# Performance work log

Measured on AMD Instinct MI355X. Metric: run time of the kernel, lower is better.

## Reference

```python
import jax, jax.numpy as jnp
import numpy as np

D = 1024
H = 16
HD = D // H
EPS = 1e-5
NEG = -1e20


def _layernorm(x, w, b):
    m = jnp.mean(x, axis=-1, keepdims=True)
    v = jnp.mean((x - m) ** 2, axis=-1, keepdims=True)
    return (x - m) * jax.lax.rsqrt(v + EPS) * w + b


def setup_inputs() -> dict:
    key = jax.random.key(0)
    ks = jax.random.split(key, 16)
    s = 0.02
    inp = {
        "X": jax.random.normal(ks[0], (2, 2048, D), jnp.float32),
        "Wq": jax.random.normal(ks[1], (D, D), jnp.float32) * s,
        "bq": jnp.zeros((D,), jnp.float32),
        "Wk": jax.random.normal(ks[2], (D, D), jnp.float32) * s,
        "bk": jnp.zeros((D,), jnp.float32),
        "Wv": jax.random.normal(ks[3], (D, D), jnp.float32) * s,
        "bv": jnp.zeros((D,), jnp.float32),
        "Wo": jax.random.normal(ks[4], (D, D), jnp.float32) * s,
        "bo": jnp.zeros((D,), jnp.float32),
        "ln1_w": jnp.ones((D,), jnp.float32),
        "ln1_b": jnp.zeros((D,), jnp.float32),
        "Wup": jax.random.normal(ks[5], (4 * D, D), jnp.float32) * s,
        "bup": jnp.zeros((4 * D,), jnp.float32),
        "Wdown": jax.random.normal(ks[6], (D, 4 * D), jnp.float32) * s,
        "bdown": jnp.zeros((D,), jnp.float32),
        "ln2_w": jnp.ones((D,), jnp.float32),
        "ln2_b": jnp.zeros((D,), jnp.float32),
    }
    return inp


def reference(X, Wq, bq, Wk, bk, Wv, bv, Wo, bo, ln1_w, ln1_b,
              Wup, bup, Wdown, bdown, ln2_w, ln2_b):
    B, S, _ = X.shape
    # QKV projections -> [B, H, S, HD]
    q = (X @ Wq.T + bq).reshape(B, S, H, HD).transpose(0, 2, 1, 3)
    k = (X @ Wk.T + bk).reshape(B, S, H, HD).transpose(0, 2, 1, 3)
    v = (X @ Wv.T + bv).reshape(B, S, H, HD).transpose(0, 2, 1, 3)
    scores = jnp.einsum("bhqd,bhkd->bhqk", q, k) / jnp.sqrt(jnp.float32(HD))
    causal = jnp.tril(jnp.ones((S, S), dtype=bool))  # mask==0 -> -1e20
    scores = jnp.where(causal, scores, jnp.float32(NEG))
    attn = jax.nn.softmax(scores, axis=-1)  # dropout is identity in eval
    out = jnp.einsum("bhqk,bhkd->bhqd", attn, v)
    out = out.transpose(0, 2, 1, 3).reshape(B, S, D)
    out = out @ Wo.T + bo
    x = _layernorm(X + out, ln1_w, ln1_b)  # post-LN attention block
    up = jax.nn.relu(x @ Wup.T + bup)
    down = up @ Wdown.T + bdown
    return _layernorm(x + down, ln2_w, ln2_b)
```

## Files before the change

### kernel.cpp

```cpp
#include <hip/hip_runtime.h>
#include <stdint.h>

#define DMODEL 1024
#define NHEAD 16
#define HDIM 64
#define SEQ 2048
#define NBATCH 2
#define MTOK 4096

typedef float f32x4 __attribute__((ext_vector_type(4)));
typedef short s16x8 __attribute__((ext_vector_type(8)));
typedef unsigned short u16;
typedef u16 u16x4 __attribute__((ext_vector_type(4)));

typedef __attribute__((address_space(1))) const void* as1_cvp;
typedef __attribute__((address_space(3))) void* as3_vp;

__device__ inline u16 f2bf(float f) {
  uint32_t u = __float_as_uint(f);
  u = u + 0x7FFFu + ((u >> 16) & 1u);
  return (u16)(u >> 16);
}

__device__ inline uint32_t pk_bf16(float lo, float hi) {
  uint32_t r;
  asm("v_cvt_pk_bf16_f32 %0, %1, %2" : "=v"(r) : "v"(lo), "v"(hi));
  return r;
}

__device__ inline void gload_lds16(const void* g, void* l) {
  __builtin_amdgcn_global_load_lds((as1_cvp)g, (as3_vp)l, 16, 0, 0);
}

__global__ __launch_bounds__(256) void k_f2bf_all(
    const float* __restrict__ X, const float* __restrict__ Wq,
    const float* __restrict__ Wk, const float* __restrict__ Wv,
    const float* __restrict__ Wo, const float* __restrict__ Wup,
    const float* __restrict__ Wdown, u16* __restrict__ dX,
    u16* __restrict__ dqkv, u16* __restrict__ dwo, u16* __restrict__ dup,
    u16* __restrict__ ddown) {
  const int c = blockIdx.y;
  const size_t CH = 1024 * 1024;
  const float* src;
  u16* dst;
  if (c < 4) {
    src = X + c * CH; dst = dX + c * CH;
  } else if (c < 7) {
    src = (c == 4 ? Wq : c == 5 ? Wk : Wv) ; dst = dqkv + (size_t)(c - 4) * CH;
  } else if (c == 7) {
    src = Wo; dst = dwo;
  } else if (c < 12) {
    src = Wup + (size_t)(c - 8) * CH; dst = dup + (size_t)(c - 8) * CH;
  } else {
    src = Wdown + (size_t)(c - 12) * CH; dst = ddown + (size_t)(c - 12) * CH;
  }
  const int n4 = (int)(CH / 4);
  int i = blockIdx.x * 256 + threadIdx.x;
  const int stride = gridDim.x * 256;
  for (; i < n4; i += stride) {
    f32x4 v = ((const f32x4*)src)[i];
    u16x4 o;
    o[0] = f2bf(v[0]); o[1] = f2bf(v[1]); o[2] = f2bf(v[2]); o[3] = f2bf(v[3]);
    ((u16x4*)dst)[i] = o;
  }
}

template <int MODE, int KSPL, int MH>
__global__ __launch_bounds__(512, 2) void k_gemm256(
    const u16* __restrict__ A, const u16* __restrict__ B,
    const float* __restrict__ bias, void* __restrict__ Cv,
    void* __restrict__ Cv1, int M, int N, int K) {
  constexpr int HALVES = MH + 2;
  __shared__ alignas(16) u16 lds[2 * HALVES * 8192];
  const int t = threadIdx.x;
  const int w = t >> 6;
  const int l = t & 63;
  const int wr = w >> 2;
  const int wc = w & 3;
  const int lr = l & 15, lg = l >> 4;
  const int r7 = lr & 7;
  const int lrow8 = l >> 3;

  const int gx = gridDim.x;
  int lin = blockIdx.y * gx + blockIdx.x;
  const int nwg = gx * gridDim.y;
  lin = (lin & 7) * (nwg >> 3) + (lin >> 3);
  const int bx = lin % gx, by = lin / gx;
  const int kz = KSPL > 1 ? blockIdx.z : 0;
  const int Kc = K / KSPL, kbeg = kz * Kc;
  const int brow = by * (MH * 128), bcol = bx * 256;

  constexpr int MF = MH * 4;
  const f32x4 Z4 = {0.f, 0.f, 0.f, 0.f};
  f32x4 acc[MF][4];
#pragma unroll
  for (int m = 0; m < MF; m++)
#pragma unroll
    for (int n = 0; n < 4; n++) acc[m][n] = Z4;

  const u16* Ag = A + (size_t)brow * K + kbeg;
  const u16* Bg = B + (size_t)bcol * K + kbeg;
  const int swz_src = ((l & 7) ^ ((l >> 3) & 7)) << 3;

  auto ldsH = [&](int buf, int half) { return lds + (buf * HALVES + half) * 8192; };
  auto stageA = [&](int kt, int buf) {
#pragma unroll
    for (int h = 0; h < MH; h++) {
      u16* lb = ldsH(buf, h);
      const int rb = h * 128;
      gload_lds16(Ag + (size_t)(rb + w * 8 + lrow8) * K + kt * 64 + swz_src,
                  lb + w * 512);
      gload_lds16(Ag + (size_t)(rb + 64 + w * 8 + lrow8) * K + kt * 64 + swz_src,
                  lb + (8 + w) * 512);
    }
  };
  auto stageB = [&](int kt, int buf) {
#pragma unroll
    for (int h = 0; h < 2; h++) {
      u16* lb = ldsH(buf, MH + h);
      const int rb = h * 128;
      gload_lds16(Bg + (size_t)(rb + w * 8 + lrow8) * K + kt * 64 + swz_src,
                  lb + w * 512);
      gload_lds16(Bg + (size_t)(rb + 64 + w * 8 + lrow8) * K + kt * 64 + swz_src,
                  lb + (8 + w) * 512);
    }
  };

  stageA(0, 0);
  stageB(0, 0);

  const int nkt = Kc >> 6;
  const int arb = (MH == 2) ? 0 : wr * 64;
  const int brb = (wc & 1) * 64;
  for (int kt = 0; kt < nkt; ++kt) {
    const int cur = kt & 1, nx = cur ^ 1;
    if (kt + 1 < nkt) {
      stageA(kt + 1, nx);
      if (MH == 2)
        asm volatile("s_waitcnt vmcnt(4)" ::: "memory");
      else
        asm volatile("s_waitcnt vmcnt(2)" ::: "memory");
    } else {
      asm volatile("s_waitcnt vmcnt(0)" ::: "memory");
    }
    __builtin_amdgcn_s_barrier();
    __builtin_amdgcn_sched_barrier(0);
    const u16* Ah = ldsH(cur, (MH == 2) ? wr : 0);
    const u16* Bh = ldsH(cur, MH + (wc >> 1));
#pragma unroll
    for (int kk = 0; kk < 2; kk++) {
      s16x8 bfr[4];
#pragma unroll
      for (int nf = 0; nf < 4; nf++)
        bfr[nf] = *(const s16x8*)(Bh + (brb + nf * 16 + lr) * 64 +
                                  (((kk * 4 + lg) ^ r7) << 3));
#pragma unroll
      for (int mh = 0; mh < MH; mh++) {
        s16x8 afr[4];
#pragma unroll
        for (int i = 0; i < 4; i++)
          afr[i] = *(const s16x8*)(Ah + (arb + (mh * 4 + i) * 16 + lr) * 64 +
                                   (((kk * 4 + lg) ^ r7) << 3));
        __builtin_amdgcn_s_setprio(1);
#pragma unroll
        for (int i = 0; i < 4; i++)
#pragma unroll
          for (int nf = 0; nf < 4; nf++)
            acc[mh * 4 + i][nf] = __builtin_amdgcn_mfma_f32_16x16x32_bf16(
                afr[i], bfr[nf], acc[mh * 4 + i][nf], 0, 0, 0);
        __builtin_amdgcn_s_setprio(0);
      }
      if (kk == 0 && kt + 1 < nkt) stageB(kt + 1, nx);
    }
    __builtin_amdgcn_sched_barrier(0);
    __builtin_amdgcn_s_barrier();
  }

  const int lg4 = lg * 4;
  const int wrb = wr * (MH == 2 ? 128 : 64);
  if (MODE == 0) {
    float* Co = (kz == 0) ? (float*)Cv : (float*)Cv1;
#pragma unroll
    for (int nf = 0; nf < 4; nf++) {
      const int col = bcol + wc * 64 + nf * 16 + lr;
      const float bvv = (kz == 0) ? bias[col] : 0.0f;
#pragma unroll
      for (int mf = 0; mf < MF; mf++) {
        const int row0 = brow + wrb + mf * 16 + lg4;
#pragma unroll
        for (int r = 0; r < 4; r++)
          Co[(size_t)(row0 + r) * N + col] = acc[mf][nf][r] + bvv;
      }
    }
  } else {
    u16* Sgw = lds + w * 2176;
    float bn[4];
#pragma unroll
    for (int nf = 0; nf < 4; nf++) bn[nf] = bias[bcol + wc * 64 + nf * 16 + lr];
    const int ch = l & 7;
#pragma unroll
    for (int hh = 0; hh < MH * 2; hh++) {
#pragma unroll
      for (int mm = 0; mm < 2; mm++) {
        const int mf = hh * 2 + mm;
#pragma unroll
        for (int nf = 0; nf < 4; nf++)
#pragma unroll
          for (int r = 0; r < 4; r++) {
            float vv = acc[mf][nf][r] + bn[nf];
            if (MODE == 2) vv = vv > 0.f ? vv : 0.f;
            Sgw[(mm * 16 + lg4 + r) * 68 + nf * 16 + lr] = f2bf(vv);
          }
      }
#pragma unroll
      for (int i = 0; i < 4; i++) {
        const int rr = i * 8 + (l >> 3);
        u16x4 a0 = *(const u16x4*)(Sgw + rr * 68 + ch * 8);
        u16x4 a1 = *(const u16x4*)(Sgw + rr * 68 + ch * 8 + 4);
        s16x8 v8;
#pragma unroll
        for (int j = 0; j < 4; j++) { v8[j] = (short)a0[j]; v8[4 + j] = (short)a1[j]; }
        *(s16x8*)((u16*)Cv + (size_t)(brow + wrb + hh * 32 + rr) * N +
                  (bcol + wc * 64 + ch * 8)) = v8;
      }
    }
  }
}

__global__ __launch_bounds__(512, 2) void k_gemm256_qkv(
    const u16* __restrict__ A, const u16* __restrict__ B,
    const float* __restrict__ bq, const float* __restrict__ bk,
    const float* __restrict__ bv, u16* __restrict__ qbf, u16* __restrict__ kbf,
    u16* __restrict__ vtbf, int M, int N, int K) {
  __shared__ alignas(16) u16 lds[2 * 4 * 8192];
  const int t = threadIdx.x;
  const int w = t >> 6, l = t & 63;
  const int wr = w >> 2, wc = w & 3;
  const int lr = l & 15, lg = l >> 4;
  const int r7 = lr & 7;
  const int lrow8 = l >> 3;

  const int gx = gridDim.x;
  int lin = blockIdx.y * gx + blockIdx.x;
  const int nwg = gx * gridDim.y;
  lin = (lin & 7) * (nwg >> 3) + (lin >> 3);
  const int bx = lin % gx, by = lin / gx;
  const int brow = by * 256, bcol = bx * 256;

  const f32x4 Z4 = {0.f, 0.f, 0.f, 0.f};
  f32x4 acc[8][4];
#pragma unroll
  for (int m = 0; m < 8; m++)
#pragma unroll
    for (int n = 0; n < 4; n++) acc[m][n] = Z4;

  const u16* Ag = A + (size_t)brow * K;
  const u16* Bg = B + (size_t)bcol * K;
  const int swz_src = ((l & 7) ^ ((l >> 3) & 7)) << 3;

  auto ldsH = [&](int buf, int half) { return lds + (buf * 4 + half) * 8192; };
  auto stageA = [&](int kt, int buf) {
#pragma unroll
    for (int h = 0; h < 2; h++) {
      u16* lb = ldsH(buf, h);
      const int rb = h * 128;
      gload_lds16(Ag + (size_t)(rb + w * 8 + lrow8) * K + kt * 64 + swz_src,
                  lb + w * 512);
      gload_lds16(Ag + (size_t)(rb + 64 + w * 8 + lrow8) * K + kt * 64 + swz_src,
                  lb + (8 + w) * 512);
    }
  };
  auto stageB = [&](int kt, int buf) {
#pragma unroll
    for (int h = 0; h < 2; h++) {
      u16* lb = ldsH(buf, 2 + h);
      const int rb = h * 128;
      gload_lds16(Bg + (size_t)(rb + w * 8 + lrow8) * K + kt * 64 + swz_src,
                  lb + w * 512);
      gload_lds16(Bg + (size_t)(rb + 64 + w * 8 + lrow8) * K + kt * 64 + swz_src,
                  lb + (8 + w) * 512);
    }
  };

  stageA(0, 0);
  stageB(0, 0);

  const int nkt = K >> 6;
  const int brb = (wc & 1) * 64;
  for (int kt = 0; kt < nkt; ++kt) {
    const int cur = kt & 1, nx = cur ^ 1;
    if (kt + 1 < nkt) {
      stageA(kt + 1, nx);
      asm volatile("s_waitcnt vmcnt(4)" ::: "memory");
    } else {
      asm volatile("s_waitcnt vmcnt(0)" ::: "memory");
    }
    __builtin_amdgcn_s_barrier();
    __builtin_amdgcn_sched_barrier(0);
    const u16* Ah = ldsH(cur, wr);
    const u16* Bh = ldsH(cur, 2 + (wc >> 1));
#pragma unroll
    for (int kk = 0; kk < 2; kk++) {
      s16x8 bfr[4];
#pragma unroll
      for (int nf = 0; nf < 4; nf++)
        bfr[nf] = *(const s16x8*)(Bh + (brb + nf * 16 + lr) * 64 +
                                  (((kk * 4 + lg) ^ r7) << 3));
#pragma unroll
      for (int mh = 0; mh < 2; mh++) {
        s16x8 afr[4];
#pragma unroll
        for (int i = 0; i < 4; i++)
          afr[i] = *(const s16x8*)(Ah + ((mh * 4 + i) * 16 + lr) * 64 +
                                   (((kk * 4 + lg) ^ r7) << 3));
        __builtin_amdgcn_s_setprio(1);
#pragma unroll
        for (int i = 0; i < 4; i++)
#pragma unroll
          for (int nf = 0; nf < 4; nf++)
            acc[mh * 4 + i][nf] = __builtin_amdgcn_mfma_f32_16x16x32_bf16(
                afr[i], bfr[nf], acc[mh * 4 + i][nf], 0, 0, 0);
        __builtin_amdgcn_s_setprio(0);
      }
      if (kk == 0 && kt + 1 < nkt) stageB(kt + 1, nx);
    }
    __builtin_amdgcn_sched_barrier(0);
    __builtin_amdgcn_s_barrier();
  }

  const int lg4 = lg * 4;
  const int wrb = wr * 128;
  u16* Sgw = lds + w * 2176;
  const int colw = bcol + wc * 64;
  const int region = colw >> 10;
  const int ck0 = colw & 1023;
  float bn[4];
  {
    const float* bb = region == 0 ? bq : region == 1 ? bk : bv;
#pragma unroll
    for (int nf = 0; nf < 4; nf++) bn[nf] = bb[ck0 + nf * 16 + lr];
  }
  const int ch = l & 7;
  if (region <= 1) {
#pragma unroll
    for (int hh = 0; hh < 4; hh++) {
#pragma unroll
      for (int mm = 0; mm < 2; mm++) {
        const int mf = hh * 2 + mm;
#pragma unroll
        for (int nf = 0; nf < 4; nf++)
#pragma unroll
          for (int r = 0; r < 4; r++) {
            float vv = acc[mf][nf][r] + bn[nf];
            if (region == 0) vv *= 0.125f;
            Sgw[(mm * 16 + lg4 + r) * 68 + nf * 16 + lr] = f2bf(vv);
          }
      }
#pragma unroll
      for (int i = 0; i < 4; i++) {
        const int rr = i * 8 + (l >> 3);
        u16x4 a0 = *(const u16x4*)(Sgw + rr * 68 + ch * 8);
        u16x4 a1 = *(const u16x4*)(Sgw + rr * 68 + ch * 8 + 4);
        s16x8 v8;
#pragma unroll
        for (int j = 0; j < 4; j++) { v8[j] = (short)a0[j]; v8[4 + j] = (short)a1[j]; }
        const int tok = brow + wrb + hh * 32 + rr;
        if (region == 0)
          *(s16x8*)(qbf + (size_t)tok * 1024 + ck0 + ch * 8) = v8;
        else
          *(s16x8*)(kbf + (size_t)tok * 1024 + ck0 + (((ch ^ tok) & 7) << 3)) =
              v8;
      }
    }
  } else {
    const int hcol = ck0 >> 6;
#pragma unroll
    for (int dh = 0; dh < 2; dh++)
#pragma unroll
      for (int th = 0; th < 2; th++) {
#pragma unroll
        for (int nn = 0; nn < 2; nn++) {
          const int nf = dh * 2 + nn;
#pragma unroll
          for (int mi = 0; mi < 4; mi++) {
            const int mf = th * 4 + mi;
#pragma unroll
            for (int r = 0; r < 4; r++)
              Sgw[(nn * 16 + lr) * 68 + mi * 16 + lg4 + r] =
                  f2bf(acc[mf][nf][r] + bn[nf]);
          }
        }
#pragma unroll
        for (int i = 0; i < 4; i++) {
          const int rr = i * 8 + (l >> 3);
          u16x4 a0 = *(const u16x4*)(Sgw + rr * 68 + ch * 8);
          u16x4 a1 = *(const u16x4*)(Sgw + rr * 68 + ch * 8 + 4);
          s16x8 v8;
#pragma unroll
          for (int j = 0; j < 4; j++) { v8[j] = (short)a0[j]; v8[4 + j] = (short)a1[j]; }
          const int d = dh * 32 + rr;
          const int tokb = brow + wrb + th * 64 + ch * 8;
          const int b = tokb >> 11, s64b = tokb & 2047;
          const int ssb = (s64b & ~63) + ((((s64b >> 3) ^ d) & 7) << 3);
          *(s16x8*)(vtbf + ((size_t)((b << 4) + hcol) * 64 + d) * 2048 + ssb) =
              v8;
        }
      }
  }
}

__global__ __launch_bounds__(512, 1) void k_attn(const u16* __restrict__ q,
                                                 const u16* __restrict__ kk,
                                                 const u16* __restrict__ vt,
                                                 u16* __restrict__ o) {
  __shared__ alignas(16) u16 Ks[2][2][64 * 64];
  __shared__ alignas(16) u16 Vs[2][2][64 * 64];
  __shared__ alignas(16) u16 Ps[8][2][16 * 64];
  const int t = threadIdx.x;
  const int w = t >> 6;
  const int l = t & 63;
  const int idx = blockIdx.x;
  const int bh = idx & 31;
  const int p = idx >> 5;
  const int b = bh >> 4, h = bh & 15;
  const u16* qb = q + (size_t)b * SEQ * DMODEL + h * HDIM;
  const u16* kb = kk + (size_t)b * SEQ * DMODEL + h * HDIM;
  const u16* vb = vt + (size_t)((b * 16 + h) * 64) * SEQ;

  const int sr = t >> 3;
  const int sc = (t & 7) * 8;
  const int lr = l & 15, lg = l >> 4;
  const int key = lr & 7;
  const f32x4 Z4 = {0.f, 0.f, 0.f, 0.f};
  u16* PsW = &Ps[0][0][0] + w * 2048;

  for (int half = 0; half < 2; half++) {
    const int qt = half ? (15 - p) : p;
    const int nt = qt + 1;
    gload_lds16(
        qb + (size_t)(qt * 128 + w * 16 + (l >> 3)) * DMODEL + (l & 7) * 8,
        PsW);
    gload_lds16(
        qb + (size_t)(qt * 128 + w * 16 + 8 + (l >> 3)) * DMODEL + (l & 7) * 8,
        PsW + 512);
#pragma unroll
    for (int s = 0; s < 2; s++) {
      gload_lds16(kb + (size_t)(s * 64 + sr) * DMODEL + sc,
                  &Ks[0][s][0] + w * 512);
      gload_lds16(vb + (size_t)sr * SEQ + s * 64 + sc, &Vs[0][s][0] + w * 512);
    }

    float m_l = -3.0e38f, l_l = 0.f;
    f32x4 oacc[4];
#pragma unroll
    for (int m = 0; m < 4; m++) oacc[m] = Z4;
    s16x8 bq0, bq1;

    for (int jt = 0; jt < nt; jt++) {
      const int cur = jt & 1;
      if (jt + 1 < nt) {
        const int nx = cur ^ 1;
        const int kvb = (jt + 1) * 128;
#pragma unroll
        for (int s = 0; s < 2; s++) {
          gload_lds16(kb + (size_t)(kvb + s * 64 + sr) * DMODEL + sc,
                      &Ks[nx][s][0] + w * 512);
          gload_lds16(vb + (size_t)sr * SEQ + kvb + s * 64 + sc,
                      &Vs[nx][s][0] + w * 512);
        }
        asm volatile("s_waitcnt vmcnt(4)" ::: "memory");
      } else {
        asm volatile("s_waitcnt vmcnt(0)" ::: "memory");
      }
      __builtin_amdgcn_s_barrier();
      __builtin_amdgcn_sched_barrier(0);
      if (jt == 0) {
        bq0 = *(const s16x8*)(PsW + lr * 64 + lg * 8);
        bq1 = *(const s16x8*)(PsW + lr * 64 + 32 + lg * 8);
      }
      f32x4 sacc[8];
#pragma unroll
      for (int m = 0; m < 8; m++) sacc[m] = Z4;
#pragma unroll
      for (int m = 0; m < 8; m++) {
        const u16* Kc = &Ks[cur][m >> 2][0];
        const int rr = (m & 3) * 16 + lr;
        s16x8 ak0 = *(const s16x8*)(Kc + rr * 64 + ((lg ^ key) << 3));
        s16x8 ak1 = *(const s16x8*)(Kc + rr * 64 + (((4 | lg) ^ key) << 3));
        sacc[m] = __builtin_amdgcn_mfma_f32_16x16x32_bf16(ak0, bq0, sacc[m], 0, 0, 0);
        sacc[m] = __builtin_amdgcn_mfma_f32_16x16x32_bf16(ak1, bq1, sacc[m], 0, 0, 0);
      }
      if (jt == nt - 1) {
        const int qg = qt * 128 + w * 16 + lr - jt * 128;
#pragma unroll
        for (int m = 0; m < 8; m++)
#pragma unroll
          for (int r = 0; r < 4; r++)
            if (m * 16 + lg * 4 + r > qg) sacc[m][r] = -3.0e38f;
      }
      float mx[8];
#pragma unroll
      for (int m = 0; m < 8; m++)
        mx[m] = fmaxf(fmaxf(sacc[m][0], sacc[m][1]),
                      fmaxf(sacc[m][2], sacc[m][3]));
      float pmax = fmaxf(fmaxf(fmaxf(mx[0], mx[1]), fmaxf(mx[2], mx[3])),
                         fmaxf(fmaxf(mx[4], mx[5]), fmaxf(mx[6], mx[7])));
      pmax = fmaxf(pmax, __shfl_xor(pmax, 16, 64));
      pmax = fmaxf(pmax, __shfl_xor(pmax, 32, 64));
      if (!__all(pmax - m_l <= 8.0f)) {
        const float m_new = fmaxf(m_l, pmax);
        const float alpha = __expf(m_l - m_new);
        m_l = m_new;
        l_l *= alpha;
#pragma unroll
        for (int m = 0; m < 4; m++)
#pragma unroll
          for (int r = 0; r < 4; r++) oacc[m][r] *= alpha;
      }
      float p_[8][4], sm[8];
#pragma unroll
      for (int m = 0; m < 8; m++) {
#pragma unroll
        for (int r = 0; r < 4; r++) p_[m][r] = __expf(sacc[m][r] - m_l);
        sm[m] = (p_[m][0] + p_[m][1]) + (p_[m][2] + p_[m][3]);
      }
      float rs = ((sm[0] + sm[1]) + (sm[2] + sm[3])) +
                 ((sm[4] + sm[5]) + (sm[6] + sm[7]));
      rs += __shfl_xor(rs, 16, 64);
      rs += __shfl_xor(rs, 32, 64);
      l_l += rs;
#pragma unroll
      for (int m = 0; m < 8; m++)
#pragma unroll
        for (int pr = 0; pr < 2; pr++) {
          const uint32_t pk = pk_bf16(p_[m][2 * pr], p_[m][2 * pr + 1]);
          const int kv0 = m * 16 + lg * 4 + 2 * pr;
          const int sub = kv0 >> 6, kvp = kv0 & 63;
          ((uint32_t*)(PsW + sub * 1024))[lr * 32 + (((kvp >> 3) ^ key) << 2) +
                                          ((kvp >> 1) & 3)] = pk;
        }
      __builtin_amdgcn_sched_barrier(0);
#pragma unroll
      for (int ks = 0; ks < 4; ks++) {
        const int sub = ks >> 1;
        const int c = (ks & 1) * 4 + lg;
        s16x8 bp =
            *(const s16x8*)(PsW + sub * 1024 + lr * 64 + ((c ^ key) << 3));
        const u16* Vc = &Vs[cur][sub][0];
#pragma unroll
        for (int m = 0; m < 4; m++) {
          s16x8 av =
              *(const s16x8*)(Vc + (m * 16 + lr) * 64 + ((c ^ key) << 3));
          oacc[m] = __builtin_amdgcn_mfma_f32_16x16x32_bf16(av, bp, oacc[m], 0, 0, 0);
        }
      }
      __builtin_amdgcn_sched_barrier(0);
      __builtin_amdgcn_s_barrier();
    }
    const float rl = 1.0f / l_l;
    const int tok = qt * 128 + w * 16 + lr;
    u16* orow = o + (size_t)(b * SEQ + tok) * DMODEL + h * HDIM;
#pragma unroll
    for (int m = 0; m < 4; m++)
#pragma unroll
      for (int pr = 0; pr < 2; pr++) {
        const uint32_t pk =
            pk_bf16(oacc[m][2 * pr] * rl, oacc[m][2 * pr + 1] * rl);
        *(uint32_t*)(orow + m * 16 + lg * 4 + 2 * pr) = pk;
      }
  }
}

template <int XBF>
__global__ __launch_bounds__(256) void k_add_ln(const void* __restrict__ Xv,
                                                const float* __restrict__ Y,
                                                const float* __restrict__ Y1,
                                                const float* __restrict__ w,
                                                const float* __restrict__ bias,
                                                float* __restrict__ of32,
                                                u16* __restrict__ obf) {
  __shared__ float sred[4];
  const int t = threadIdx.x;
  const size_t row = blockIdx.x;
  f32x4 xv;
  if (XBF) {
    u16x4 xu = ((const u16x4*)((const u16*)Xv + row * DMODEL))[t];
    for (int i = 0; i < 4; i++)
      xv[i] = __uint_as_float((uint32_t)xu[i] << 16);
  } else {
    xv = ((const f32x4*)((const float*)Xv + row * DMODEL))[t];
  }
  f32x4 yv = ((const f32x4*)(Y + row * DMODEL))[t];
  f32x4 vv;
  for (int i = 0; i < 4; i++) vv[i] = xv[i] + yv[i];
  if (Y1) {
    f32x4 y1 = ((const f32x4*)(Y1 + row * DMODEL))[t];
    for (int i = 0; i < 4; i++) vv[i] += y1[i];
  }
  float s = vv[0] + vv[1] + vv[2] + vv[3];
  for (int off = 32; off >= 1; off >>= 1) s += __shfl_xor(s, off, 64);
  if ((t & 63) == 0) sred[t >> 6] = s;
  __syncthreads();
  s = sred[0] + sred[1] + sred[2] + sred[3];
  const float mean = s * (1.0f / DMODEL);
  f32x4 dv;
  for (int i = 0; i < 4; i++) dv[i] = vv[i] - mean;
  float ss = dv[0] * dv[0] + dv[1] * dv[1] + dv[2] * dv[2] + dv[3] * dv[3];
  __syncthreads();
  for (int off = 32; off >= 1; off >>= 1) ss += __shfl_xor(ss, off, 64);
  if ((t & 63) == 0) sred[t >> 6] = ss;
  __syncthreads();
  ss = sred[0] + sred[1] + sred[2] + sred[3];
  const float rs = rsqrtf(ss * (1.0f / DMODEL) + 1e-5f);
  f32x4 wv = ((const f32x4*)w)[t];
  f32x4 bv = ((const f32x4*)bias)[t];
  f32x4 ov;
  for (int i = 0; i < 4; i++) ov[i] = dv[i] * rs * wv[i] + bv[i];
  if (of32) ((f32x4*)(of32 + row * DMODEL))[t] = ov;
  if (obf) {
    u16x4 ob;
    for (int i = 0; i < 4; i++) ob[i] = f2bf(ov[i]);
    ((u16x4*)(obf + row * DMODEL))[t] = ob;
  }
}

extern "C" void kernel_launch(void* const* d_in, const int* in_sizes, int n_in,
                              void* d_out, int out_size, void* d_ws,
                              size_t ws_size, hipStream_t stream) {
  const float* X = (const float*)d_in[0];
  const float* Wq = (const float*)d_in[1];
  const float* bq = (const float*)d_in[2];
  const float* Wk = (const float*)d_in[3];
  const float* bk = (const float*)d_in[4];
  const float* Wv = (const float*)d_in[5];
  const float* bvp = (const float*)d_in[6];
  const float* Wo = (const float*)d_in[7];
  const float* bo = (const float*)d_in[8];
  const float* ln1w = (const float*)d_in[9];
  const float* ln1b = (const float*)d_in[10];
  const float* Wup = (const float*)d_in[11];
  const float* bup = (const float*)d_in[12];
  const float* Wdown = (const float*)d_in[13];
  const float* bdown = (const float*)d_in[14];
  const float* ln2w = (const float*)d_in[15];
  const float* ln2b = (const float*)d_in[16];

  char* ws = (char*)d_ws;
  const size_t MB = 1024 * 1024;
  u16* Xbf = (u16*)(ws + 0);
  u16* qbf = (u16*)(ws + 8 * MB);
  u16* kbf = (u16*)(ws + 16 * MB);
  u16* vtbf = (u16*)(ws + 24 * MB);
  u16* wqkv = (u16*)(ws + 32 * MB);
  u16* wo = (u16*)(ws + 38 * MB);
  u16* attnb = (u16*)(ws + 40 * MB);
  float* Ybuf = (float*)(ws + 48 * MB);
  u16* wbig = (u16*)(ws + 64 * MB);
  u16* wdownbf = (u16*)(ws + 72 * MB);
  u16* xbf = (u16*)(ws + 80 * MB);
  u16* upbf = (u16*)(ws + 0);
  float* Ypart = (float*)d_out;

  const dim3 blk(256);
  k_f2bf_all<<<dim3(128, 16), blk, 0, stream>>>(
      X, Wq, Wk, Wv, Wo, Wup, Wdown, Xbf, wqkv, wo, wbig, wdownbf);

  k_gemm256_qkv<<<dim3(12, 16), dim3(512), 0, stream>>>(
      Xbf, wqkv, bq, bk, bvp, qbf, kbf, vtbf, MTOK, 3 * DMODEL, DMODEL);
  k_attn<<<8 * NBATCH * NHEAD, dim3(512), 0, stream>>>(qbf, kbf, vtbf, attnb);
  k_gemm256<0, 2, 1><<<dim3(4, 32, 2), dim3(512), 0, stream>>>(
      attnb, wo, bo, Ybuf, Ypart, MTOK, DMODEL, DMODEL);
  k_add_ln<0><<<MTOK, blk, 0, stream>>>(X, Ybuf, Ypart, ln1w, ln1b,
                                        (float*)nullptr, xbf);

  k_gemm256<2, 1, 2><<<dim3(16, 16), dim3(512), 0, stream>>>(
      xbf, wbig, bup, upbf, nullptr, MTOK, 4 * DMODEL, DMODEL);
  k_gemm256<0, 2, 1><<<dim3(4, 32, 2), dim3(512), 0, stream>>>(
      upbf, wdownbf, bdown, Ybuf, Ypart, MTOK, DMODEL, 4 * DMODEL);
  k_add_ln<1><<<MTOK, blk, 0, stream>>>(xbf, Ybuf, Ypart, ln2w, ln2b,
                                        (float*)d_out, (u16*)nullptr);
}
```

Baseline: 196.1 us.

## Split attention blocks per query tile and halve P scratch for two blocks per CU

Each attention block used to process a pair of query tiles (p and 15-p) to balance causal work. It now handles a single query tile, and the grid doubles to 512 blocks, with block order interleaving short and long tiles. The per-wave P scratch in LDS is halved by writing and consuming P one 64-key sub-tile at a time, and the launch bounds now request two blocks per CU to raise occupancy. In exchange, per-block load balance comes from the scheduler instead of explicit pairing, and the lower register budget may cause spills.

```diff
diff --git a/kernel.cpp b/kernel.cpp
--- a/kernel.cpp
+++ b/kernel.cpp
@@ -409,19 +409,21 @@
   }
 }
 
-__global__ __launch_bounds__(512, 1) void k_attn(const u16* __restrict__ q,
+__global__ __launch_bounds__(512, 2) void k_attn(const u16* __restrict__ q,
                                                  const u16* __restrict__ kk,
                                                  const u16* __restrict__ vt,
                                                  u16* __restrict__ o) {
   __shared__ alignas(16) u16 Ks[2][2][64 * 64];
   __shared__ alignas(16) u16 Vs[2][2][64 * 64];
-  __shared__ alignas(16) u16 Ps[8][2][16 * 64];
+  __shared__ alignas(16) u16 Ps[8][16 * 64];
   const int t = threadIdx.x;
   const int w = t >> 6;
   const int l = t & 63;
   const int idx = blockIdx.x;
   const int bh = idx & 31;
-  const int p = idx >> 5;
+  const int pp = idx >> 5;
+  const int qt = (pp < 8) ? pp : (23 - pp);
+  const int nt = qt + 1;
   const int b = bh >> 4, h = bh & 15;
   const u16* qb = q + (size_t)b * SEQ * DMODEL + h * HDIM;
   const u16* kb = kk + (size_t)b * SEQ * DMODEL + h * HDIM;
@@ -432,121 +434,118 @@
   const int lr = l & 15, lg = l >> 4;
   const int key = lr & 7;
   const f32x4 Z4 = {0.f, 0.f, 0.f, 0.f};
-  u16* PsW = &Ps[0][0][0] + w * 2048;
-
-  for (int half = 0; half < 2; half++) {
-    const int qt = half ? (15 - p) : p;
-    const int nt = qt + 1;
-    gload_lds16(
-        qb + (size_t)(qt * 128 + w * 16 + (l >> 3)) * DMODEL + (l & 7) * 8,
-        PsW);
-    gload_lds16(
-        qb + (size_t)(qt * 128 + w * 16 + 8 + (l >> 3)) * DMODEL + (l & 7) * 8,
-        PsW + 512);
-#pragma unroll
-    for (int s = 0; s < 2; s++) {
-      gload_lds16(kb + (size_t)(s * 64 + sr) * DMODEL + sc,
-                  &Ks[0][s][0] + w * 512);
-      gload_lds16(vb + (size_t)sr * SEQ + s * 64 + sc, &Vs[0][s][0] + w * 512);
-    }
-
-    float m_l = -3.0e38f, l_l = 0.f;
-    f32x4 oacc[4];
-#pragma unroll
-    for (int m = 0; m < 4; m++) oacc[m] = Z4;
-    s16x8 bq0, bq1;
-
-    for (int jt = 0; jt < nt; jt++) {
-      const int cur = jt & 1;
-      if (jt + 1 < nt) {
-        const int nx = cur ^ 1;
-        const int kvb = (jt + 1) * 128;
-#pragma unroll
-        for (int s = 0; s < 2; s++) {
-          gload_lds16(kb + (size_t)(kvb + s * 64 + sr) * DMODEL + sc,
-                      &Ks[nx][s][0] + w * 512);
-          gload_lds16(vb + (size_t)sr * SEQ + kvb + s * 64 + sc,
-                      &Vs[nx][s][0] + w * 512);
-        }
-        asm volatile("s_waitcnt vmcnt(4)" ::: "memory");
-      } else {
-        asm volatile("s_waitcnt vmcnt(0)" ::: "memory");
-      }
-      __builtin_amdgcn_s_barrier();
-      __builtin_amdgcn_sched_barrier(0);
-      if (jt == 0) {
-        bq0 = *(const s16x8*)(PsW + lr * 64 + lg * 8);
-        bq1 = *(const s16x8*)(PsW + lr * 64 + 32 + lg * 8);
-      }
-      f32x4 sacc[8];
-#pragma unroll
-      for (int m = 0; m < 8; m++) sacc[m] = Z4;
-#pragma unroll
-      for (int m = 0; m < 8; m++) {
-        const u16* Kc = &Ks[cur][m >> 2][0];
-        const int rr = (m & 3) * 16 + lr;
-        s16x8 ak0 = *(const s16x8*)(Kc + rr * 64 + ((lg ^ key) << 3));
-        s16x8 ak1 = *(const s16x8*)(Kc + rr * 64 + (((4 | lg) ^ key) << 3));
-        sacc[m] = __builtin_amdgcn_mfma_f32_16x16x32_bf16(ak0, bq0, sacc[m], 0, 0, 0);
-        sacc[m] = __builtin_amdgcn_mfma_f32_16x16x32_bf16(ak1, bq1, sacc[m], 0, 0, 0);
-      }
-      if (jt == nt - 1) {
-        const int qg = qt * 128 + w * 16 + lr - jt * 128;
-#pragma unroll
-        for (int m = 0; m < 8; m++)
-#pragma unroll
-          for (int r = 0; r < 4; r++)
-            if (m * 16 + lg * 4 + r > qg) sacc[m][r] = -3.0e38f;
-      }
-      float mx[8];
+  u16* PsW = &Ps[0][0] + w * 1024;
+
+  gload_lds16(
+      qb + (size_t)(qt * 128 + w * 16 + (l >> 3)) * DMODEL + (l & 7) * 8, PsW);
+  gload_lds16(
+      qb + (size_t)(qt * 128 + w * 16 + 8 + (l >> 3)) * DMODEL + (l & 7) * 8,
+      PsW + 512);
+#pragma unroll
+  for (int s = 0; s < 2; s++) {
+    gload_lds16(kb + (size_t)(s * 64 + sr) * DMODEL + sc,
+                &Ks[0][s][0] + w * 512);
+    gload_lds16(vb + (size_t)sr * SEQ + s * 64 + sc, &Vs[0][s][0] + w * 512);
+  }
+
+  float m_l = -3.0e38f, l_l = 0.f;
+  f32x4 oacc[4];
+#pragma unroll
+  for (int m = 0; m < 4; m++) oacc[m] = Z4;
+  s16x8 bq0, bq1;
+
+  for (int jt = 0; jt < nt; jt++) {
+    const int cur = jt & 1;
+    if (jt + 1 < nt) {
+      const int nx = cur ^ 1;
+      const int kvb = (jt + 1) * 128;
+#pragma unroll
+      for (int s = 0; s < 2; s++) {
+        gload_lds16(kb + (size_t)(kvb + s * 64 + sr) * DMODEL + sc,
+                    &Ks[nx][s][0] + w * 512);
+        gload_lds16(vb + (size_t)sr * SEQ + kvb + s * 64 + sc,
+                    &Vs[nx][s][0] + w * 512);
+      }
+      asm volatile("s_waitcnt vmcnt(4)" ::: "memory");
+    } else {
+      asm volatile("s_waitcnt vmcnt(0)" ::: "memory");
+    }
+    __builtin_amdgcn_s_barrier();
+    __builtin_amdgcn_sched_barrier(0);
+    if (jt == 0) {
+      bq0 = *(const s16x8*)(PsW + lr * 64 + lg * 8);
+      bq1 = *(const s16x8*)(PsW + lr * 64 + 32 + lg * 8);
+    }
+    f32x4 sacc[8];
+#pragma unroll
+    for (int m = 0; m < 8; m++) sacc[m] = Z4;
+#pragma unroll
+    for (int m = 0; m < 8; m++) {
+      const u16* Kc = &Ks[cur][m >> 2][0];
+      const int rr = (m & 3) * 16 + lr;
+      s16x8 ak0 = *(const s16x8*)(Kc + rr * 64 + ((lg ^ key) << 3));
+      s16x8 ak1 = *(const s16x8*)(Kc + rr * 64 + (((4 | lg) ^ key) << 3));
+      sacc[m] = __builtin_amdgcn_mfma_f32_16x16x32_bf16(ak0, bq0, sacc[m], 0, 0, 0);
+      sacc[m] = __builtin_amdgcn_mfma_f32_16x16x32_bf16(ak1, bq1, sacc[m], 0, 0, 0);
+    }
+    if (jt == nt - 1) {
+      const int qg = w * 16 + lr;
 #pragma unroll
       for (int m = 0; m < 8; m++)
-        mx[m] = fmaxf(fmaxf(sacc[m][0], sacc[m][1]),
-                      fmaxf(sacc[m][2], sacc[m][3]));
-      float pmax = fmaxf(fmaxf(fmaxf(mx[0], mx[1]), fmaxf(mx[2], mx[3])),
-                         fmaxf(fmaxf(mx[4], mx[5]), fmaxf(mx[6], mx[7])));
-      pmax = fmaxf(pmax, __shfl_xor(pmax, 16, 64));
-      pmax = fmaxf(pmax, __shfl_xor(pmax, 32, 64));
-      if (!__all(pmax - m_l <= 8.0f)) {
-        const float m_new = fmaxf(m_l, pmax);
-        const float alpha = __expf(m_l - m_new);
-        m_l = m_new;
-        l_l *= alpha;
-#pragma unroll
-        for (int m = 0; m < 4; m++)
-#pragma unroll
-          for (int r = 0; r < 4; r++) oacc[m][r] *= alpha;
-      }
-      float p_[8][4], sm[8];
-#pragma unroll
-      for (int m = 0; m < 8; m++) {
-#pragma unroll
-        for (int r = 0; r < 4; r++) p_[m][r] = __expf(sacc[m][r] - m_l);
-        sm[m] = (p_[m][0] + p_[m][1]) + (p_[m][2] + p_[m][3]);
-      }
-      float rs = ((sm[0] + sm[1]) + (sm[2] + sm[3])) +
-                 ((sm[4] + sm[5]) + (sm[6] + sm[7]));
-      rs += __shfl_xor(rs, 16, 64);
-      rs += __shfl_xor(rs, 32, 64);
-      l_l += rs;
-#pragma unroll
-      for (int m = 0; m < 8; m++)
+#pragma unroll
+        for (int r = 0; r < 4; r++)
+          if (m * 16 + lg * 4 + r > qg) sacc[m][r] = -3.0e38f;
+    }
+    float mx[8];
+#pragma unroll
+    for (int m = 0; m < 8; m++)
+      mx[m] = fmaxf(fmaxf(sacc[m][0], sacc[m][1]),
+                    fmaxf(sacc[m][2], sacc[m][3]));
+    float pmax = fmaxf(fmaxf(fmaxf(mx[0], mx[1]), fmaxf(mx[2], mx[3])),
+                       fmaxf(fmaxf(mx[4], mx[5]), fmaxf(mx[6], mx[7])));
+    pmax = fmaxf(pmax, __shfl_xor(pmax, 16, 64));
+    pmax = fmaxf(pmax, __shfl_xor(pmax, 32, 64));
+    if (!__all(pmax - m_l <= 8.0f)) {
+      const float m_new = fmaxf(m_l, pmax);
+      const float alpha = __expf(m_l - m_new);
+      m_l = m_new;
+      l_l *= alpha;
+#pragma unroll
+      for (int m = 0; m < 4; m++)
+#pragma unroll
+        for (int r = 0; r < 4; r++) oacc[m][r] *= alpha;
+    }
+    float p_[8][4], sm[8];
+#pragma unroll
+    for (int m = 0; m < 8; m++) {
+#pragma unroll
+      for (int r = 0; r < 4; r++) p_[m][r] = __expf(sacc[m][r] - m_l);
+      sm[m] = (p_[m][0] + p_[m][1]) + (p_[m][2] + p_[m][3]);
+    }
+    float rs = ((sm[0] + sm[1]) + (sm[2] + sm[3])) +
+               ((sm[4] + sm[5]) + (sm[6] + sm[7]));
+    rs += __shfl_xor(rs, 16, 64);
+    rs += __shfl_xor(rs, 32, 64);
+    l_l += rs;
+#pragma unroll
+    for (int sub = 0; sub < 2; sub++) {
+#pragma unroll
+      for (int mi = 0; mi < 4; mi++) {
+        const int m = sub * 4 + mi;
 #pragma unroll
         for (int pr = 0; pr < 2; pr++) {
           const uint32_t pk = pk_bf16(p_[m][2 * pr], p_[m][2 * pr + 1]);
-          const int kv0 = m * 16 + lg * 4 + 2 * pr;
-          const int sub = kv0 >> 6, kvp = kv0 & 63;
-          ((uint32_t*)(PsW + sub * 1024))[lr * 32 + (((kvp >> 3) ^ key) << 2) +
-                                          ((kvp >> 1) & 3)] = pk;
+          const int kvp = mi * 16 + lg * 4 + 2 * pr;
+          ((uint32_t*)PsW)[lr * 32 + (((kvp >> 3) ^ key) << 2) +
+                           ((kvp >> 1) & 3)] = pk;
         }
+      }
       __builtin_amdgcn_sched_barrier(0);
-#pragma unroll
-      for (int ks = 0; ks < 4; ks++) {
-        const int sub = ks >> 1;
-        const int c = (ks & 1) * 4 + lg;
-        s16x8 bp =
-            *(const s16x8*)(PsW + sub * 1024 + lr * 64 + ((c ^ key) << 3));
-        const u16* Vc = &Vs[cur][sub][0];
+      const u16* Vc = &Vs[cur][sub][0];
+#pragma unroll
+      for (int ki = 0; ki < 2; ki++) {
+        const int c = ki * 4 + lg;
+        s16x8 bp = *(const s16x8*)(PsW + lr * 64 + ((c ^ key) << 3));
 #pragma unroll
         for (int m = 0; m < 4; m++) {
           s16x8 av =
@@ -555,20 +554,20 @@
         }
       }
       __builtin_amdgcn_sched_barrier(0);
-      __builtin_amdgcn_s_barrier();
-    }
-    const float rl = 1.0f / l_l;
-    const int tok = qt * 128 + w * 16 + lr;
-    u16* orow = o + (size_t)(b * SEQ + tok) * DMODEL + h * HDIM;
-#pragma unroll
-    for (int m = 0; m < 4; m++)
-#pragma unroll
-      for (int pr = 0; pr < 2; pr++) {
-        const uint32_t pk =
-            pk_bf16(oacc[m][2 * pr] * rl, oacc[m][2 * pr + 1] * rl);
-        *(uint32_t*)(orow + m * 16 + lg * 4 + 2 * pr) = pk;
-      }
-  }
+    }
+    __builtin_amdgcn_s_barrier();
+  }
+  const float rl = 1.0f / l_l;
+  const int tok = qt * 128 + w * 16 + lr;
+  u16* orow = o + (size_t)(b * SEQ + tok) * DMODEL + h * HDIM;
+#pragma unroll
+  for (int m = 0; m < 4; m++)
+#pragma unroll
+    for (int pr = 0; pr < 2; pr++) {
+      const uint32_t pk =
+          pk_bf16(oacc[m][2 * pr] * rl, oacc[m][2 * pr + 1] * rl);
+      *(uint32_t*)(orow + m * 16 + lg * 4 + 2 * pr) = pk;
+    }
 }
 
 template <int XBF>
@@ -667,7 +666,7 @@
 
   k_gemm256_qkv<<<dim3(12, 16), dim3(512), 0, stream>>>(
       Xbf, wqkv, bq, bk, bvp, qbf, kbf, vtbf, MTOK, 3 * DMODEL, DMODEL);
-  k_attn<<<8 * NBATCH * NHEAD, dim3(512), 0, stream>>>(qbf, kbf, vtbf, attnb);
+  k_attn<<<16 * NBATCH * NHEAD, dim3(512), 0, stream>>>(qbf, kbf, vtbf, attnb);
   k_gemm256<0, 2, 1><<<dim3(4, 32, 2), dim3(512), 0, stream>>>(
       attnb, wo, bo, Ybuf, Ypart, MTOK, DMODEL, DMODEL);
   k_add_ln<0><<<MTOK, blk, 0, stream>>>(X, Ybuf, Ypart, ln1w, ln1b,
```

Result: no change. 195.3 us (median of 2 runs) (-0.4%).

## Restructure attention to small blocks reading K/V directly from global memory

Applied to the files above, without the earlier changes.

Rewrites the attention kernel to use 256-thread blocks with 64-row query tiles. Each block handles one query tile instead of pairing two, with a new tile ordering meant to balance the causal work. K and V are no longer staged through double-buffered shared memory; each wave loads its MFMA operands straight from global memory and relies on cache. This removes the barriers and shared-memory traffic and raises occupancy to four blocks per CU. The swizzled layouts in the QKV epilogue are dropped to match, at the risk of redundant global and L2 traffic, since each wave rereads the same K/V rows.

```diff
diff --git a/kernel.cpp b/kernel.cpp
--- a/kernel.cpp
+++ b/kernel.cpp
@@ -365,11 +365,8 @@
 #pragma unroll
         for (int j = 0; j < 4; j++) { v8[j] = (short)a0[j]; v8[4 + j] = (short)a1[j]; }
         const int tok = brow + wrb + hh * 32 + rr;
-        if (region == 0)
-          *(s16x8*)(qbf + (size_t)tok * 1024 + ck0 + ch * 8) = v8;
-        else
-          *(s16x8*)(kbf + (size_t)tok * 1024 + ck0 + (((ch ^ tok) & 7) << 3)) =
-              v8;
+        u16* dstp = (region == 0) ? qbf : kbf;
+        *(s16x8*)(dstp + (size_t)tok * 1024 + ck0 + ch * 8) = v8;
       }
     }
   } else {
@@ -401,174 +398,127 @@
           const int d = dh * 32 + rr;
           const int tokb = brow + wrb + th * 64 + ch * 8;
           const int b = tokb >> 11, s64b = tokb & 2047;
-          const int ssb = (s64b & ~63) + ((((s64b >> 3) ^ d) & 7) << 3);
-          *(s16x8*)(vtbf + ((size_t)((b << 4) + hcol) * 64 + d) * 2048 + ssb) =
+          *(s16x8*)(vtbf + ((size_t)((b << 4) + hcol) * 64 + d) * 2048 + s64b) =
               v8;
         }
       }
   }
 }
 
-__global__ __launch_bounds__(512, 1) void k_attn(const u16* __restrict__ q,
+__global__ __launch_bounds__(256, 4) void k_attn(const u16* __restrict__ q,
                                                  const u16* __restrict__ kk,
                                                  const u16* __restrict__ vt,
                                                  u16* __restrict__ o) {
-  __shared__ alignas(16) u16 Ks[2][2][64 * 64];
-  __shared__ alignas(16) u16 Vs[2][2][64 * 64];
-  __shared__ alignas(16) u16 Ps[8][2][16 * 64];
+  __shared__ alignas(16) u16 Ps[4][16 * 64];
   const int t = threadIdx.x;
   const int w = t >> 6;
   const int l = t & 63;
   const int idx = blockIdx.x;
   const int bh = idx & 31;
   const int p = idx >> 5;
+  const int pm = p >> 3, pj = p & 7;
+  const int qt = pm * 8 + ((pm & 1) ? (7 - pj) : pj);
+  const int nt = qt + 1;
   const int b = bh >> 4, h = bh & 15;
   const u16* qb = q + (size_t)b * SEQ * DMODEL + h * HDIM;
   const u16* kb = kk + (size_t)b * SEQ * DMODEL + h * HDIM;
-  const u16* vb = vt + (size_t)((b * 16 + h) * 64) * SEQ;
-
-  const int sr = t >> 3;
-  const int sc = (t & 7) * 8;
+  const u16* vb = vt + (size_t)(bh * 64) * SEQ;
   const int lr = l & 15, lg = l >> 4;
   const int key = lr & 7;
   const f32x4 Z4 = {0.f, 0.f, 0.f, 0.f};
-  u16* PsW = &Ps[0][0][0] + w * 2048;
-
-  for (int half = 0; half < 2; half++) {
-    const int qt = half ? (15 - p) : p;
-    const int nt = qt + 1;
-    gload_lds16(
-        qb + (size_t)(qt * 128 + w * 16 + (l >> 3)) * DMODEL + (l & 7) * 8,
-        PsW);
-    gload_lds16(
-        qb + (size_t)(qt * 128 + w * 16 + 8 + (l >> 3)) * DMODEL + (l & 7) * 8,
-        PsW + 512);
-#pragma unroll
-    for (int s = 0; s < 2; s++) {
-      gload_lds16(kb + (size_t)(s * 64 + sr) * DMODEL + sc,
-                  &Ks[0][s][0] + w * 512);
-      gload_lds16(vb + (size_t)sr * SEQ + s * 64 + sc, &Vs[0][s][0] + w * 512);
-    }
-
-    float m_l = -3.0e38f, l_l = 0.f;
-    f32x4 oacc[4];
-#pragma unroll
-    for (int m = 0; m < 4; m++) oacc[m] = Z4;
-    s16x8 bq0, bq1;
-
-    for (int jt = 0; jt < nt; jt++) {
-      const int cur = jt & 1;
-      if (jt + 1 < nt) {
-        const int nx = cur ^ 1;
-        const int kvb = (jt + 1) * 128;
-#pragma unroll
-        for (int s = 0; s < 2; s++) {
-          gload_lds16(kb + (size_t)(kvb + s * 64 + sr) * DMODEL + sc,
-                      &Ks[nx][s][0] + w * 512);
-          gload_lds16(vb + (size_t)sr * SEQ + kvb + s * 64 + sc,
-                      &Vs[nx][s][0] + w * 512);
-        }
-        asm volatile("s_waitcnt vmcnt(4)" ::: "memory");
-      } else {
-        asm volatile("s_waitcnt vmcnt(0)" ::: "memory");
-      }
-      __builtin_amdgcn_s_barrier();
-      __builtin_amdgcn_sched_barrier(0);
-      if (jt == 0) {
-        bq0 = *(const s16x8*)(PsW + lr * 64 + lg * 8);
-        bq1 = *(const s16x8*)(PsW + lr * 64 + 32 + lg * 8);
-      }
-      f32x4 sacc[8];
-#pragma unroll
-      for (int m = 0; m < 8; m++) sacc[m] = Z4;
-#pragma unroll
-      for (int m = 0; m < 8; m++) {
-        const u16* Kc = &Ks[cur][m >> 2][0];
-        const int rr = (m & 3) * 16 + lr;
-        s16x8 ak0 = *(const s16x8*)(Kc + rr * 64 + ((lg ^ key) << 3));
-        s16x8 ak1 = *(const s16x8*)(Kc + rr * 64 + (((4 | lg) ^ key) << 3));
-        sacc[m] = __builtin_amdgcn_mfma_f32_16x16x32_bf16(ak0, bq0, sacc[m], 0, 0, 0);
-        sacc[m] = __builtin_amdgcn_mfma_f32_16x16x32_bf16(ak1, bq1, sacc[m], 0, 0, 0);
-      }
-      if (jt == nt - 1) {
-        const int qg = qt * 128 + w * 16 + lr - jt * 128;
-#pragma unroll
-        for (int m = 0; m < 8; m++)
-#pragma unroll
-          for (int r = 0; r < 4; r++)
-            if (m * 16 + lg * 4 + r > qg) sacc[m][r] = -3.0e38f;
-      }
-      float mx[8];
-#pragma unroll
-      for (int m = 0; m < 8; m++)
-        mx[m] = fmaxf(fmaxf(sacc[m][0], sacc[m][1]),
-                      fmaxf(sacc[m][2], sacc[m][3]));
-      float pmax = fmaxf(fmaxf(fmaxf(mx[0], mx[1]), fmaxf(mx[2], mx[3])),
-                         fmaxf(fmaxf(mx[4], mx[5]), fmaxf(mx[6], mx[7])));
-      pmax = fmaxf(pmax, __shfl_xor(pmax, 16, 64));
-      pmax = fmaxf(pmax, __shfl_xor(pmax, 32, 64));
-      if (!__all(pmax - m_l <= 8.0f)) {
-        const float m_new = fmaxf(m_l, pmax);
-        const float alpha = __expf(m_l - m_new);
-        m_l = m_new;
-        l_l *= alpha;
-#pragma unroll
-        for (int m = 0; m < 4; m++)
-#pragma unroll
-          for (int r = 0; r < 4; r++) oacc[m][r] *= alpha;
-      }
-      float p_[8][4], sm[8];
-#pragma unroll
-      for (int m = 0; m < 8; m++) {
-#pragma unroll
-        for (int r = 0; r < 4; r++) p_[m][r] = __expf(sacc[m][r] - m_l);
-        sm[m] = (p_[m][0] + p_[m][1]) + (p_[m][2] + p_[m][3]);
-      }
-      float rs = ((sm[0] + sm[1]) + (sm[2] + sm[3])) +
-                 ((sm[4] + sm[5]) + (sm[6] + sm[7]));
-      rs += __shfl_xor(rs, 16, 64);
-      rs += __shfl_xor(rs, 32, 64);
-      l_l += rs;
-#pragma unroll
-      for (int m = 0; m < 8; m++)
-#pragma unroll
-        for (int pr = 0; pr < 2; pr++) {
-          const uint32_t pk = pk_bf16(p_[m][2 * pr], p_[m][2 * pr + 1]);
-          const int kv0 = m * 16 + lg * 4 + 2 * pr;
-          const int sub = kv0 >> 6, kvp = kv0 & 63;
-          ((uint32_t*)(PsW + sub * 1024))[lr * 32 + (((kvp >> 3) ^ key) << 2) +
-                                          ((kvp >> 1) & 3)] = pk;
-        }
-      __builtin_amdgcn_sched_barrier(0);
-#pragma unroll
-      for (int ks = 0; ks < 4; ks++) {
-        const int sub = ks >> 1;
-        const int c = (ks & 1) * 4 + lg;
-        s16x8 bp =
-            *(const s16x8*)(PsW + sub * 1024 + lr * 64 + ((c ^ key) << 3));
-        const u16* Vc = &Vs[cur][sub][0];
-#pragma unroll
-        for (int m = 0; m < 4; m++) {
-          s16x8 av =
-              *(const s16x8*)(Vc + (m * 16 + lr) * 64 + ((c ^ key) << 3));
-          oacc[m] = __builtin_amdgcn_mfma_f32_16x16x32_bf16(av, bp, oacc[m], 0, 0, 0);
-        }
-      }
-      __builtin_amdgcn_sched_barrier(0);
-      __builtin_amdgcn_s_barrier();
-    }
-    const float rl = 1.0f / l_l;
-    const int tok = qt * 128 + w * 16 + lr;
-    u16* orow = o + (size_t)(b * SEQ + tok) * DMODEL + h * HDIM;
+  u16* PsW = &Ps[w][0];
+
+  const int qrow = qt * 64 + w * 16 + lr;
+  const u16* qrp = qb + (size_t)qrow * DMODEL + lg * 8;
+  s16x8 bq0 = *(const s16x8*)(qrp);
+  s16x8 bq1 = *(const s16x8*)(qrp + 32);
+
+  float m_l = -3.0e38f, l_l = 0.f;
+  f32x4 oacc[4];
+#pragma unroll
+  for (int m = 0; m < 4; m++) oacc[m] = Z4;
+
+  for (int jt = 0; jt < nt; jt++) {
+    f32x4 sacc[4];
+#pragma unroll
+    for (int m = 0; m < 4; m++) sacc[m] = Z4;
+#pragma unroll
+    for (int m = 0; m < 4; m++) {
+      const u16* kr = kb + (size_t)(jt * 64 + m * 16 + lr) * DMODEL + lg * 8;
+      s16x8 ak0 = *(const s16x8*)(kr);
+      s16x8 ak1 = *(const s16x8*)(kr + 32);
+      sacc[m] = __builtin_amdgcn_mfma_f32_16x16x32_bf16(ak0, bq0, sacc[m], 0, 0, 0);
+      sacc[m] = __builtin_amdgcn_mfma_f32_16x16x32_bf16(ak1, bq1, sacc[m], 0, 0, 0);
+    }
+    if (jt == qt) {
+      const int q_rel = w * 16 + lr;
+#pragma unroll
+      for (int m = 0; m < 4; m++)
+#pragma unroll
+        for (int r = 0; r < 4; r++)
+          if (m * 16 + lg * 4 + r > q_rel) sacc[m][r] = -3.0e38f;
+    }
+    float mx[4];
 #pragma unroll
     for (int m = 0; m < 4; m++)
+      mx[m] = fmaxf(fmaxf(sacc[m][0], sacc[m][1]),
+                    fmaxf(sacc[m][2], sacc[m][3]));
+    float pmax = fmaxf(fmaxf(mx[0], mx[1]), fmaxf(mx[2], mx[3]));
+    pmax = fmaxf(pmax, __shfl_xor(pmax, 16, 64));
+    pmax = fmaxf(pmax, __shfl_xor(pmax, 32, 64));
+    if (!__all(pmax - m_l <= 8.0f)) {
+      const float m_new = fmaxf(m_l, pmax);
+      const float alpha = __expf(m_l - m_new);
+      m_l = m_new;
+      l_l *= alpha;
+#pragma unroll
+      for (int m = 0; m < 4; m++)
+#pragma unroll
+        for (int r = 0; r < 4; r++) oacc[m][r] *= alpha;
+    }
+    float p_[4][4], sm[4];
+#pragma unroll
+    for (int m = 0; m < 4; m++) {
+#pragma unroll
+      for (int r = 0; r < 4; r++) p_[m][r] = __expf(sacc[m][r] - m_l);
+      sm[m] = (p_[m][0] + p_[m][1]) + (p_[m][2] + p_[m][3]);
+    }
+    float rs = (sm[0] + sm[1]) + (sm[2] + sm[3]);
+    rs += __shfl_xor(rs, 16, 64);
+    rs += __shfl_xor(rs, 32, 64);
+    l_l += rs;
+#pragma unroll
+    for (int m = 0; m < 4; m++)
 #pragma unroll
       for (int pr = 0; pr < 2; pr++) {
-        const uint32_t pk =
-            pk_bf16(oacc[m][2 * pr] * rl, oacc[m][2 * pr + 1] * rl);
-        *(uint32_t*)(orow + m * 16 + lg * 4 + 2 * pr) = pk;
-      }
-  }
+        const uint32_t pk = pk_bf16(p_[m][2 * pr], p_[m][2 * pr + 1]);
+        const int kv0 = m * 16 + lg * 4 + 2 * pr;
+        ((uint32_t*)PsW)[lr * 32 + (((kv0 >> 3) ^ key) << 2) +
+                         ((kv0 >> 1) & 3)] = pk;
+      }
+    __builtin_amdgcn_sched_barrier(0);
+    s16x8 bp0 = *(const s16x8*)(PsW + lr * 64 + ((lg ^ key) << 3));
+    s16x8 bp1 = *(const s16x8*)(PsW + lr * 64 + (((4 | lg) ^ key) << 3));
+#pragma unroll
+    for (int m = 0; m < 4; m++) {
+      const u16* vr = vb + (size_t)(m * 16 + lr) * SEQ + jt * 64 + lg * 8;
+      s16x8 av0 = *(const s16x8*)(vr);
+      s16x8 av1 = *(const s16x8*)(vr + 32);
+      oacc[m] = __builtin_amdgcn_mfma_f32_16x16x32_bf16(av0, bp0, oacc[m], 0, 0, 0);
+      oacc[m] = __builtin_amdgcn_mfma_f32_16x16x32_bf16(av1, bp1, oacc[m], 0, 0, 0);
+    }
+    __builtin_amdgcn_sched_barrier(0);
+  }
+  const float rl = 1.0f / l_l;
+  u16* orow = o + (size_t)(b * SEQ + qrow) * DMODEL + h * HDIM;
+#pragma unroll
+  for (int m = 0; m < 4; m++)
+#pragma unroll
+    for (int pr = 0; pr < 2; pr++) {
+      const uint32_t pk =
+          pk_bf16(oacc[m][2 * pr] * rl, oacc[m][2 * pr + 1] * rl);
+      *(uint32_t*)(orow + m * 16 + lg * 4 + 2 * pr) = pk;
+    }
 }
 
 template <int XBF>
@@ -667,7 +617,7 @@
 
   k_gemm256_qkv<<<dim3(12, 16), dim3(512), 0, stream>>>(
       Xbf, wqkv, bq, bk, bvp, qbf, kbf, vtbf, MTOK, 3 * DMODEL, DMODEL);
-  k_attn<<<8 * NBATCH * NHEAD, dim3(512), 0, stream>>>(qbf, kbf, vtbf, attnb);
+  k_attn<<<32 * NBATCH * NHEAD, blk, 0, stream>>>(qbf, kbf, vtbf, attnb);
   k_gemm256<0, 2, 1><<<dim3(4, 32, 2), dim3(512), 0, stream>>>(
       attnb, wo, bo, Ybuf, Ypart, MTOK, DMODEL, DMODEL);
   k_add_ln<0><<<MTOK, blk, 0, stream>>>(X, Ybuf, Ypart, ln1w, ln1b,
```

New measurement: 278.1 us. 41.8% more time.
